# Performance work log

Hardware: AMD Instinct MI355X
Metric: run time of the kernel (lower is better)

## Reference

```python
import jax, jax.numpy as jnp
import numpy as np

E = 8          # num_experts
K = 2          # top_k
D = 1024       # hidden_size
I = 4096       # intermediate_size
AUX_COEF = 0.02


def setup_inputs() -> dict:
    key = jax.random.key(0)
    ks = jax.random.split(key, 5)
    x = jax.random.normal(ks[0], (4, 2048, D), dtype=jnp.float32)
    w_gate = jax.random.normal(ks[1], (E, D), dtype=jnp.float32) * 0.02   # router, nn.Linear weight [E, D]
    wg = jax.random.normal(ks[2], (E, D, I), dtype=jnp.float32) * 0.02    # gate_proj per expert
    wu = jax.random.normal(ks[3], (E, D, I), dtype=jnp.float32) * 0.02    # up_proj per expert
    wd = jax.random.normal(ks[4], (E, I, D), dtype=jnp.float32) * 0.02    # down_proj per expert
    return {"x": x, "w_gate": w_gate, "wg": wg, "wu": wu, "wd": wd}


def reference(x, w_gate, wg, wu, wd):
    B, T, Dm = x.shape
    xf = x.reshape(-1, Dm)                                   # [N, D]
    N = xf.shape[0]

    # 1) Router: softmax (in fp32) + top-k, renormalize top-k weights
    logits = xf @ w_gate.T                                   # [N, E]
    probs = jax.nn.softmax(logits.astype(jnp.float32), axis=-1)
    topk_w, topk_idx = jax.lax.top_k(probs, K)               # [N, K]
    topk_w = (topk_w / topk_w.sum(-1, keepdims=True)).astype(x.dtype)

    # Per-expert combine weight (zero when expert not selected) — math-equivalent
    # to the original gather/scatter-add loop but jit-friendly and vectorized.
    onehot = jax.nn.one_hot(topk_idx, E, dtype=x.dtype)      # [N, K, E]
    combine = jnp.einsum('nk,nke->ne', topk_w, onehot)       # [N, E]

    # 2) Experts: SwiGLU FFN, combined with routing weights
    out = jnp.zeros_like(xf)
    for e in range(E):  # fixed small loop over structurally distinct experts
        h = jax.nn.silu(xf @ wg[e]) * (xf @ wu[e])           # [N, I]
        out = out + combine[:, e:e + 1] * (h @ wd[e])        # [N, D]

    # 3) Load-balancing aux loss (Switch Transformer)
    f = onehot.sum((0, 1)).astype(jnp.float32) / (N * K)     # dispatch fraction per expert
    p = probs.mean(0)                                        # mean routing prob per expert
    aux_loss = AUX_COEF * E * jnp.sum(f * p)

    return out.reshape(B, T, Dm), aux_loss
```

## Files before the change

### kernel.cpp

```cpp
#include <hip/hip_runtime.h>
#include <hip/hip_bf16.h>
#include <cstdint>
#include <cstddef>

#define NE 8
#define TK 2
#define DM 1024
#define IM 4096
#define NT 8192
#define NS (NT*TK)
#define SCAP (NS+128)

typedef __bf16 bf16_t;
typedef __bf16 bf16x8 __attribute__((ext_vector_type(8)));
typedef __bf16 bf16x4 __attribute__((ext_vector_type(4)));
typedef float f32x4 __attribute__((ext_vector_type(4)));

__device__ __forceinline__ void async_cp16(const bf16_t* g, bf16_t* l) {
  __builtin_amdgcn_global_load_lds(
      (__attribute__((address_space(1))) void*)(const_cast<bf16_t*>(g)),
      (__attribute__((address_space(3))) void*)(l), 16, 0, 0);
}

__global__ void transpose_cvt(const float* __restrict__ src, bf16_t* __restrict__ dst,
                              int R, int C) {
  __shared__ float t[32][33];
  int bx = blockIdx.x * 32, by = blockIdx.y * 32;
  size_t zb = (size_t)blockIdx.z * R * C;
  int tx = threadIdx.x, ty = threadIdx.y;
#pragma unroll
  for (int i = 0; i < 4; ++i)
    t[ty + i*8][tx] = src[zb + (size_t)(by + ty + i*8) * C + bx + tx];
  __syncthreads();
#pragma unroll
  for (int i = 0; i < 4; ++i)
    dst[zb + (size_t)(bx + ty + i*8) * R + by + tx] = (bf16_t)t[tx][ty + i*8];
}

__global__ void router_kernel(const float* __restrict__ x, const float* __restrict__ wgate,
                              int* __restrict__ counts, float* __restrict__ prob_sum,
                              int* __restrict__ topk_idx, float* __restrict__ topk_w) {
  __shared__ float s_psum[NE];
  __shared__ int s_cnt[NE];
  int tid = threadIdx.x;
  if (tid < NE) { s_psum[tid] = 0.f; s_cnt[tid] = 0; }
  __syncthreads();
  int lane = tid & 63, wv = tid >> 6;
  for (int t = 0; t < 8; ++t) {
    int n = blockIdx.x * 32 + wv * 8 + t;
    float acc[NE];
#pragma unroll
    for (int e = 0; e < NE; ++e) acc[e] = 0.f;
#pragma unroll
    for (int j = 0; j < 16; ++j) {
      int d = j * 64 + lane;
      float xv = x[(size_t)n * DM + d];
#pragma unroll
      for (int e = 0; e < NE; ++e) acc[e] += xv * wgate[e * DM + d];
    }
#pragma unroll
    for (int e = 0; e < NE; ++e) {
#pragma unroll
      for (int off = 32; off > 0; off >>= 1) acc[e] += __shfl_xor(acc[e], off);
    }
    if (lane == 0) {
      float mx = acc[0];
#pragma unroll
      for (int e = 1; e < NE; ++e) mx = fmaxf(mx, acc[e]);
      float p[NE], s = 0.f;
#pragma unroll
      for (int e = 0; e < NE; ++e) { p[e] = __expf(acc[e] - mx); s += p[e]; }
      float inv = 1.f / s;
#pragma unroll
      for (int e = 0; e < NE; ++e) p[e] *= inv;
      int i0 = 0;
      for (int e = 1; e < NE; ++e) if (p[e] > p[i0]) i0 = e;
      int i1 = (i0 == 0) ? 1 : 0;
      for (int e = 0; e < NE; ++e) if (e != i0 && p[e] > p[i1]) i1 = e;
      float rs = 1.f / (p[i0] + p[i1]);
      topk_idx[n * 2 + 0] = i0; topk_idx[n * 2 + 1] = i1;
      topk_w[n * 2 + 0] = p[i0] * rs; topk_w[n * 2 + 1] = p[i1] * rs;
      atomicAdd(&s_cnt[i0], 1); atomicAdd(&s_cnt[i1], 1);
#pragma unroll
      for (int e = 0; e < NE; ++e) atomicAdd(&s_psum[e], p[e]);
    }
  }
  __syncthreads();
  if (tid < NE) { atomicAdd(&counts[tid], s_cnt[tid]); atomicAdd(&prob_sum[tid], s_psum[tid]); }
}

__global__ void scan_aux(const int* __restrict__ counts, const float* __restrict__ prob_sum,
                         int* __restrict__ offsets, int* __restrict__ cursors,
                         float* __restrict__ aux_out) {
  if (threadIdx.x == 0) {
    int off = 0;
    float aux = 0.f;
    for (int e = 0; e < NE; ++e) {
      offsets[e] = off; cursors[e] = off;
      float f = (float)counts[e] * (1.f / (float)NS);
      float p = prob_sum[e] * (1.f / (float)NT);
      aux += f * p;
      off += counts[e];
    }
    offsets[NE] = off;
    *aux_out = 0.02f * 8.f * aux;
  }
}

__global__ void gather_kernel(const float* __restrict__ x, const int* __restrict__ topk_idx,
                              const float* __restrict__ topk_w, int* __restrict__ cursors,
                              int* __restrict__ slot_token, float* __restrict__ slot_w,
                              int* __restrict__ pair_slot, bf16_t* __restrict__ Xg) {
  int lane = threadIdx.x & 63, wv = threadIdx.x >> 6;
  int pair = blockIdx.x * 4 + wv;
  int n = pair >> 1, k = pair & 1;
  int e = topk_idx[n * 2 + k];
  int slot = 0;
  if (lane == 0) slot = atomicAdd(&cursors[e], 1);
  slot = __shfl(slot, 0);
  if (lane == 0) {
    slot_token[slot] = n; slot_w[slot] = topk_w[n * 2 + k];
    pair_slot[pair] = slot;
  }
#pragma unroll
  for (int j = 0; j < 16; ++j) {
    int d = j * 64 + lane;
    Xg[(size_t)slot * DM + d] = (bf16_t)x[(size_t)n * DM + d];
  }
}

__global__ __launch_bounds__(256, 2) void gemm1_kernel(
    const bf16_t* __restrict__ Xg, const bf16_t* __restrict__ Wgt,
    const bf16_t* __restrict__ Wut, bf16_t* __restrict__ H,
    const int* __restrict__ offsets) {
  int e = blockIdx.z, mt = blockIdx.y, nt = blockIdx.x;
  int row0 = offsets[e], ne = offsets[e + 1] - row0;
  if (mt * 128 >= ne) return;
  int m0 = row0 + mt * 128;
  int n0 = nt * 128;

  __shared__ bf16_t sA[128 * 64];
  __shared__ bf16_t sG[128 * 64];
  __shared__ bf16_t sU[128 * 64];

  int tid = threadIdx.x, lane = tid & 63, wv = tid >> 6;
  int fm = lane & 15, fq = lane >> 4;
  int wm = (wv & 1) * 64, wn = (wv >> 1) * 64;

  f32x4 accg[4][4], accu[4][4];
#pragma unroll
  for (int i = 0; i < 4; ++i)
#pragma unroll
    for (int j = 0; j < 4; ++j) {
      accg[i][j] = (f32x4){0.f, 0.f, 0.f, 0.f};
      accu[i][j] = (f32x4){0.f, 0.f, 0.f, 0.f};
    }

  const bf16_t* Ab = Xg + (size_t)m0 * DM;
  const bf16_t* Gb = Wgt + ((size_t)e * IM + n0) * DM;
  const bf16_t* Ub = Wut + ((size_t)e * IM + n0) * DM;

  for (int k0 = 0; k0 < DM; k0 += 64) {
    __syncthreads();
#pragma unroll
    for (int it = 0; it < 4; ++it) {
      int c = it * 256 + tid;
      int r = c >> 3, c8 = c & 7;
      int gc8 = c8 ^ (r & 7);
      size_t go = (size_t)r * DM + k0 + gc8 * 8;
      async_cp16(Ab + go, sA + c * 8);
      async_cp16(Gb + go, sG + c * 8);
      async_cp16(Ub + go, sU + c * 8);
    }
    __syncthreads();
#pragma unroll
    for (int s = 0; s < 2; ++s) {
      bf16x8 af[4], gf[4], uf[4];
      int q = s * 4 + fq;
#pragma unroll
      for (int i = 0; i < 4; ++i) {
        int ra = wm + i * 16 + fm;
        int rb = wn + i * 16 + fm;
        af[i] = *(const bf16x8*)(sA + ra * 64 + (q ^ (ra & 7)) * 8);
        gf[i] = *(const bf16x8*)(sG + rb * 64 + (q ^ (rb & 7)) * 8);
        uf[i] = *(const bf16x8*)(sU + rb * 64 + (q ^ (rb & 7)) * 8);
      }
#pragma unroll
      for (int i = 0; i < 4; ++i)
#pragma unroll
        for (int j = 0; j < 4; ++j) {
          accg[i][j] = __builtin_amdgcn_mfma_f32_16x16x32_bf16(af[i], gf[j], accg[i][j], 0, 0, 0);
          accu[i][j] = __builtin_amdgcn_mfma_f32_16x16x32_bf16(af[i], uf[j], accu[i][j], 0, 0, 0);
        }
    }
  }
#pragma unroll
  for (int i = 0; i < 4; ++i) {
#pragma unroll
    for (int r = 0; r < 4; ++r) {
      int lm = wm + i * 16 + fq * 4 + r;
      if (mt * 128 + lm < ne) {
        bf16_t* hrow = H + (size_t)(m0 + lm) * IM + n0 + wn;
#pragma unroll
        for (int j = 0; j < 4; ++j) {
          float g = accg[i][j][r], u = accu[i][j][r];
          float h = g * __builtin_amdgcn_rcpf(1.f + __expf(-g)) * u;
          hrow[j * 16 + fm] = (bf16_t)h;
        }
      }
    }
  }
}

__global__ __launch_bounds__(256, 2) void gemm2_kernel(
    const bf16_t* __restrict__ H, const bf16_t* __restrict__ Wdt,
    const int* __restrict__ offsets, bf16_t* __restrict__ Y) {
  int e = blockIdx.z, mt = blockIdx.y, nt = blockIdx.x;
  int row0 = offsets[e], ne = offsets[e + 1] - row0;
  if (mt * 128 >= ne) return;
  int m0 = row0 + mt * 128;
  int n0 = nt * 128;

  __shared__ bf16_t sA[128 * 64];
  __shared__ bf16_t sB[128 * 64];

  int tid = threadIdx.x, lane = tid & 63, wv = tid >> 6;
  int fm = lane & 15, fq = lane >> 4;
  int wm = (wv & 1) * 64, wn = (wv >> 1) * 64;

  f32x4 acc[4][4];
#pragma unroll
  for (int i = 0; i < 4; ++i)
#pragma unroll
    for (int j = 0; j < 4; ++j) acc[i][j] = (f32x4){0.f, 0.f, 0.f, 0.f};

  const bf16_t* Ab = H + (size_t)m0 * IM;
  const bf16_t* Bb = Wdt + ((size_t)e * DM + n0) * IM;

  for (int k0 = 0; k0 < IM; k0 += 64) {
    __syncthreads();
#pragma unroll
    for (int it = 0; it < 4; ++it) {
      int c = it * 256 + tid;
      int r = c >> 3, c8 = c & 7;
      int gc8 = c8 ^ (r & 7);
      size_t go = (size_t)r * IM + k0 + gc8 * 8;
      async_cp16(Ab + go, sA + c * 8);
      async_cp16(Bb + go, sB + c * 8);
    }
    __syncthreads();
#pragma unroll
    for (int s = 0; s < 2; ++s) {
      bf16x8 af[4], bf[4];
      int q = s * 4 + fq;
#pragma unroll
      for (int i = 0; i < 4; ++i) {
        int ra = wm + i * 16 + fm;
        int rb = wn + i * 16 + fm;
        af[i] = *(const bf16x8*)(sA + ra * 64 + (q ^ (ra & 7)) * 8);
        bf[i] = *(const bf16x8*)(sB + rb * 64 + (q ^ (rb & 7)) * 8);
      }
#pragma unroll
      for (int i = 0; i < 4; ++i)
#pragma unroll
        for (int j = 0; j < 4; ++j)
          acc[i][j] = __builtin_amdgcn_mfma_f32_16x16x32_bf16(af[i], bf[j], acc[i][j], 0, 0, 0);
    }
  }
#pragma unroll
  for (int i = 0; i < 4; ++i) {
#pragma unroll
    for (int r = 0; r < 4; ++r) {
      int lm = wm + i * 16 + fq * 4 + r;
      if (mt * 128 + lm < ne) {
        bf16_t* yrow = Y + (size_t)(m0 + lm) * DM + n0 + wn;
#pragma unroll
        for (int j = 0; j < 4; ++j)
          yrow[j * 16 + fm] = (bf16_t)acc[i][j][r];
      }
    }
  }
}

__global__ void combine_kernel(const bf16_t* __restrict__ Y, const int* __restrict__ pair_slot,
                               const float* __restrict__ topk_w, float* __restrict__ out) {
  int n = blockIdx.x;
  int t = threadIdx.x;
  int s0 = pair_slot[n * 2 + 0], s1 = pair_slot[n * 2 + 1];
  float w0 = topk_w[n * 2 + 0], w1 = topk_w[n * 2 + 1];
  bf16x4 y0 = *(const bf16x4*)(Y + (size_t)s0 * DM + t * 4);
  bf16x4 y1 = *(const bf16x4*)(Y + (size_t)s1 * DM + t * 4);
  float4 o;
  o.x = w0 * (float)y0[0] + w1 * (float)y1[0];
  o.y = w0 * (float)y0[1] + w1 * (float)y1[1];
  o.z = w0 * (float)y0[2] + w1 * (float)y1[2];
  o.w = w0 * (float)y0[3] + w1 * (float)y1[3];
  *(float4*)(out + (size_t)n * DM + t * 4) = o;
}

static constexpr size_t OFF_TOPKI = 256;
static constexpr size_t OFF_TOPKW = OFF_TOPKI + (size_t)NT * 2 * 4;
static constexpr size_t OFF_STOK  = OFF_TOPKW + (size_t)NT * 2 * 4;
static constexpr size_t OFF_SW    = OFF_STOK + (size_t)NS * 4;
static constexpr size_t OFF_PSLOT = OFF_SW + (size_t)NS * 4;
static constexpr size_t OFF_XG    = OFF_PSLOT + (size_t)NS * 4;
static constexpr size_t OFF_H     = OFF_XG + (size_t)SCAP * DM * 2;
static constexpr size_t OFF_WGT   = OFF_H + (size_t)SCAP * IM * 2;
static constexpr size_t OFF_WUT   = OFF_WGT + (size_t)NE * IM * DM * 2;
static constexpr size_t OFF_WDT   = OFF_WUT + (size_t)NE * IM * DM * 2;

extern "C" void kernel_launch(void* const* d_in, const int* in_sizes, int n_in,
                              void* d_out, int out_size, void* d_ws, size_t ws_size,
                              hipStream_t stream) {
  const float* x      = (const float*)d_in[0];
  const float* w_gate = (const float*)d_in[1];
  const float* wg     = (const float*)d_in[2];
  const float* wu     = (const float*)d_in[3];
  const float* wd     = (const float*)d_in[4];
  float* out = (float*)d_out;

  char* ws = (char*)d_ws;
  int*   counts   = (int*)(ws + 0);
  int*   cursors  = (int*)(ws + 32);
  int*   offsets  = (int*)(ws + 64);
  float* prob_sum = (float*)(ws + 128);
  int*   topk_idx = (int*)(ws + OFF_TOPKI);
  float* topk_w   = (float*)(ws + OFF_TOPKW);
  int*   slot_tok = (int*)(ws + OFF_STOK);
  float* slot_w   = (float*)(ws + OFF_SW);
  int*   pair_slot= (int*)(ws + OFF_PSLOT);
  bf16_t* Xg  = (bf16_t*)(ws + OFF_XG);
  bf16_t* Yb  = Xg;
  bf16_t* Hb  = (bf16_t*)(ws + OFF_H);
  bf16_t* Wgt = (bf16_t*)(ws + OFF_WGT);
  bf16_t* Wut = (bf16_t*)(ws + OFF_WUT);
  bf16_t* Wdt = (bf16_t*)(ws + OFF_WDT);

  hipMemsetAsync(ws, 0, 256, stream);

  transpose_cvt<<<dim3(IM / 32, DM / 32, NE), dim3(32, 8), 0, stream>>>(wg, Wgt, DM, IM);
  transpose_cvt<<<dim3(IM / 32, DM / 32, NE), dim3(32, 8), 0, stream>>>(wu, Wut, DM, IM);
  transpose_cvt<<<dim3(DM / 32, IM / 32, NE), dim3(32, 8), 0, stream>>>(wd, Wdt, IM, DM);

  router_kernel<<<NT / 32, 256, 0, stream>>>(x, w_gate, counts, prob_sum, topk_idx, topk_w);
  scan_aux<<<1, 64, 0, stream>>>(counts, prob_sum, offsets, cursors, out + (out_size - 1));
  gather_kernel<<<NS / 4, 256, 0, stream>>>(x, topk_idx, topk_w, cursors, slot_tok, slot_w,
                                            pair_slot, Xg);

  gemm1_kernel<<<dim3(IM / 128, 64, NE), 256, 0, stream>>>(Xg, Wgt, Wut, Hb, offsets);
  gemm2_kernel<<<dim3(DM / 128, 64, NE), 256, 0, stream>>>(Hb, Wdt, offsets, Yb);
  combine_kernel<<<NT, 256, 0, stream>>>(Yb, pair_slot, topk_w, out);
}
```

Before: 1.241 ms.

## Rewrite gate/up GEMM as 256x256 double-buffered 8-wave kernel with packed weights

Gate and up weights are packed into one interleaved bf16 matrix, so each 256-column B tile holds 128 gate and 128 up columns. The gate/up GEMM now uses 512 threads, 256x256 tiles, double-buffered LDS, async global-to-LDS staging and explicit waitcnt, barrier and setprio scheduling to overlap loads with MFMA. The gather kernel also switches to float4 vectorized loads. Exchanges: a large LDS footprint (128 KB) that limits occupancy, more hand-tuned synchronization risk, and a 64-row grid dimension that still launches many empty blocks.

```diff
diff --git a/kernel.cpp b/kernel.cpp
--- a/kernel.cpp
+++ b/kernel.cpp
@@ -9,7 +9,7 @@
 #define IM 4096
 #define NT 8192
 #define NS (NT*TK)
-#define SCAP (NS+128)
+#define SCAP (NS+256)
 
 typedef __bf16 bf16_t;
 typedef __bf16 bf16x8 __attribute__((ext_vector_type(8)));
@@ -35,6 +35,26 @@
 #pragma unroll
   for (int i = 0; i < 4; ++i)
     dst[zb + (size_t)(bx + ty + i*8) * R + by + tx] = (bf16_t)t[tx][ty + i*8];
+}
+
+__global__ void pack_gu(const float* __restrict__ wg, const float* __restrict__ wu,
+                        bf16_t* __restrict__ Wgu) {
+  __shared__ float t[32][33];
+  int sel = blockIdx.z & 1, e = blockIdx.z >> 1;
+  const float* src = sel ? wu : wg;
+  size_t zb = (size_t)e * DM * IM;
+  int bx = blockIdx.x * 32, by = blockIdx.y * 32;
+  int tx = threadIdx.x, ty = threadIdx.y;
+#pragma unroll
+  for (int i = 0; i < 4; ++i)
+    t[ty + i*8][tx] = src[zb + (size_t)(by + ty + i*8) * IM + bx + tx];
+  __syncthreads();
+#pragma unroll
+  for (int i = 0; i < 4; ++i) {
+    int icol = bx + ty + i*8;
+    int p = ((icol >> 6) << 7) + (sel << 6) + (icol & 63);
+    Wgu[((size_t)e * (2*IM) + p) * DM + by + tx] = (bf16_t)t[tx][ty + i*8];
+  }
 }
 
 __global__ void router_kernel(const float* __restrict__ x, const float* __restrict__ wgate,
@@ -123,90 +143,174 @@
     pair_slot[pair] = slot;
   }
 #pragma unroll
-  for (int j = 0; j < 16; ++j) {
-    int d = j * 64 + lane;
-    Xg[(size_t)slot * DM + d] = (bf16_t)x[(size_t)n * DM + d];
-  }
-}
-
-__global__ __launch_bounds__(256, 2) void gemm1_kernel(
-    const bf16_t* __restrict__ Xg, const bf16_t* __restrict__ Wgt,
-    const bf16_t* __restrict__ Wut, bf16_t* __restrict__ H,
-    const int* __restrict__ offsets) {
+  for (int j = 0; j < 4; ++j) {
+    int d4 = j * 256 + lane * 4;
+    float4 v = *(const float4*)(x + (size_t)n * DM + d4);
+    bf16x4 o;
+    o[0] = (bf16_t)v.x; o[1] = (bf16_t)v.y; o[2] = (bf16_t)v.z; o[3] = (bf16_t)v.w;
+    *(bf16x4*)(Xg + (size_t)slot * DM + d4) = o;
+  }
+}
+
+#define MFMA16 __builtin_amdgcn_mfma_f32_16x16x32_bf16
+
+__global__ __launch_bounds__(512, 2) void gemm1_kernel(
+    const bf16_t* __restrict__ Xg, const bf16_t* __restrict__ Wgu,
+    bf16_t* __restrict__ H, const int* __restrict__ offsets) {
   int e = blockIdx.z, mt = blockIdx.y, nt = blockIdx.x;
   int row0 = offsets[e], ne = offsets[e + 1] - row0;
-  if (mt * 128 >= ne) return;
-  int m0 = row0 + mt * 128;
-  int n0 = nt * 128;
-
-  __shared__ bf16_t sA[128 * 64];
-  __shared__ bf16_t sG[128 * 64];
-  __shared__ bf16_t sU[128 * 64];
+  if (mt * 256 >= ne) return;
+  int m0 = row0 + mt * 256;
+
+  __shared__ bf16_t lds[2][4][128 * 64];
 
   int tid = threadIdx.x, lane = tid & 63, wv = tid >> 6;
   int fm = lane & 15, fq = lane >> 4;
-  int wm = (wv & 1) * 64, wn = (wv >> 1) * 64;
-
-  f32x4 accg[4][4], accu[4][4];
-#pragma unroll
-  for (int i = 0; i < 4; ++i)
-#pragma unroll
-    for (int j = 0; j < 4; ++j) {
-      accg[i][j] = (f32x4){0.f, 0.f, 0.f, 0.f};
-      accu[i][j] = (f32x4){0.f, 0.f, 0.f, 0.f};
-    }
+  int wm = wv >> 2, wn = wv & 3;
 
   const bf16_t* Ab = Xg + (size_t)m0 * DM;
-  const bf16_t* Gb = Wgt + ((size_t)e * IM + n0) * DM;
-  const bf16_t* Ub = Wut + ((size_t)e * IM + n0) * DM;
-
-  for (int k0 = 0; k0 < DM; k0 += 64) {
-    __syncthreads();
-#pragma unroll
-    for (int it = 0; it < 4; ++it) {
-      int c = it * 256 + tid;
-      int r = c >> 3, c8 = c & 7;
-      int gc8 = c8 ^ (r & 7);
-      size_t go = (size_t)r * DM + k0 + gc8 * 8;
-      async_cp16(Ab + go, sA + c * 8);
-      async_cp16(Gb + go, sG + c * 8);
-      async_cp16(Ub + go, sU + c * 8);
-    }
-    __syncthreads();
-#pragma unroll
-    for (int s = 0; s < 2; ++s) {
-      bf16x8 af[4], gf[4], uf[4];
-      int q = s * 4 + fq;
-#pragma unroll
-      for (int i = 0; i < 4; ++i) {
-        int ra = wm + i * 16 + fm;
-        int rb = wn + i * 16 + fm;
-        af[i] = *(const bf16x8*)(sA + ra * 64 + (q ^ (ra & 7)) * 8);
-        gf[i] = *(const bf16x8*)(sG + rb * 64 + (q ^ (rb & 7)) * 8);
-        uf[i] = *(const bf16x8*)(sU + rb * 64 + (q ^ (rb & 7)) * 8);
-      }
-#pragma unroll
-      for (int i = 0; i < 4; ++i)
-#pragma unroll
-        for (int j = 0; j < 4; ++j) {
-          accg[i][j] = __builtin_amdgcn_mfma_f32_16x16x32_bf16(af[i], gf[j], accg[i][j], 0, 0, 0);
-          accu[i][j] = __builtin_amdgcn_mfma_f32_16x16x32_bf16(af[i], uf[j], accu[i][j], 0, 0, 0);
-        }
-    }
-  }
-#pragma unroll
-  for (int i = 0; i < 4; ++i) {
-#pragma unroll
-    for (int r = 0; r < 4; ++r) {
-      int lm = wm + i * 16 + fq * 4 + r;
-      if (mt * 128 + lm < ne) {
-        bf16_t* hrow = H + (size_t)(m0 + lm) * IM + n0 + wn;
-#pragma unroll
-        for (int j = 0; j < 4; ++j) {
-          float g = accg[i][j][r], u = accu[i][j][r];
-          float h = g * __builtin_amdgcn_rcpf(1.f + __expf(-g)) * u;
-          hrow[j * 16 + fm] = (bf16_t)h;
-        }
+  const bf16_t* Bb = Wgu + ((size_t)e * (2 * IM) + nt * 256) * DM;
+
+  int sr = tid >> 3;
+  int sgc = ((tid & 7) ^ (sr & 7)) << 3;
+  int sldo = tid * 8;
+
+#define STAGE1(LDST, GBASE, COL) do {                                      \
+    const bf16_t* _g = (GBASE);                                            \
+    async_cp16(_g + (size_t)sr * DM + (COL) + sgc, (LDST) + sldo);         \
+    async_cp16(_g + (size_t)(sr + 64) * DM + (COL) + sgc, (LDST) + sldo + 4096); \
+  } while (0)
+
+  int offA[4][2], offB[2][2];
+#pragma unroll
+  for (int m = 0; m < 4; ++m) {
+    int r = m * 32 + wm * 16 + fm;
+#pragma unroll
+    for (int ks = 0; ks < 2; ++ks)
+      offA[m][ks] = r * 64 + (((ks * 4 + fq) ^ (r & 7)) << 3);
+  }
+#pragma unroll
+  for (int jh = 0; jh < 2; ++jh) {
+    int r = jh * 64 + wn * 16 + fm;
+#pragma unroll
+    for (int ks = 0; ks < 2; ++ks)
+      offB[jh][ks] = r * 64 + (((ks * 4 + fq) ^ (r & 7)) << 3);
+  }
+
+  f32x4 acc[8][4];
+#pragma unroll
+  for (int i = 0; i < 8; ++i)
+#pragma unroll
+    for (int j = 0; j < 4; ++j) acc[i][j] = (f32x4){0.f, 0.f, 0.f, 0.f};
+
+  STAGE1(lds[0][0], Ab, 0);
+  STAGE1(lds[0][2], Bb, 0);
+  STAGE1(lds[0][3], Bb + (size_t)128 * DM, 0);
+  STAGE1(lds[0][1], Ab + (size_t)128 * DM, 0);
+  STAGE1(lds[1][0], Ab, 64);
+  STAGE1(lds[1][2], Bb, 64);
+  STAGE1(lds[1][3], Bb + (size_t)128 * DM, 64);
+  asm volatile("s_waitcnt vmcnt(6)");
+  __builtin_amdgcn_s_barrier();
+
+  bf16x8 af[4][2], b0f[2][2], b1f[2][2];
+#pragma unroll 1
+  for (int t = 0; t < 16; ++t) {
+    const int buf = t & 1;
+    const bf16_t* LA0 = lds[buf][0];
+    const bf16_t* LA1 = lds[buf][1];
+    const bf16_t* LB0 = lds[buf][2];
+    const bf16_t* LB1 = lds[buf][3];
+#pragma unroll
+    for (int m = 0; m < 4; ++m) {
+      af[m][0] = *(const bf16x8*)(LA0 + offA[m][0]);
+      af[m][1] = *(const bf16x8*)(LA0 + offA[m][1]);
+    }
+#pragma unroll
+    for (int j = 0; j < 2; ++j) {
+      b0f[j][0] = *(const bf16x8*)(LB0 + offB[j][0]);
+      b0f[j][1] = *(const bf16x8*)(LB0 + offB[j][1]);
+    }
+    if (t + 1 < 16) STAGE1(lds[buf ^ 1][1], Ab + (size_t)128 * DM, (t + 1) * 64);
+    __builtin_amdgcn_s_barrier();
+    asm volatile("s_waitcnt lgkmcnt(0)");
+    __builtin_amdgcn_sched_barrier(0);
+    __builtin_amdgcn_s_setprio(1);
+#pragma unroll
+    for (int m = 0; m < 4; ++m)
+#pragma unroll
+      for (int j = 0; j < 2; ++j) {
+        acc[m][j] = MFMA16(af[m][0], b0f[j][0], acc[m][j], 0, 0, 0);
+        acc[m][j] = MFMA16(af[m][1], b0f[j][1], acc[m][j], 0, 0, 0);
+      }
+    __builtin_amdgcn_s_setprio(0);
+    __builtin_amdgcn_s_barrier();
+#pragma unroll
+    for (int j = 0; j < 2; ++j) {
+      b1f[j][0] = *(const bf16x8*)(LB1 + offB[j][0]);
+      b1f[j][1] = *(const bf16x8*)(LB1 + offB[j][1]);
+    }
+    if (t + 2 < 16) STAGE1(lds[buf][0], Ab, (t + 2) * 64);
+    __builtin_amdgcn_s_barrier();
+    asm volatile("s_waitcnt lgkmcnt(0)");
+    __builtin_amdgcn_sched_barrier(0);
+    __builtin_amdgcn_s_setprio(1);
+#pragma unroll
+    for (int m = 0; m < 4; ++m)
+#pragma unroll
+      for (int j = 0; j < 2; ++j) {
+        acc[m][2 + j] = MFMA16(af[m][0], b1f[j][0], acc[m][2 + j], 0, 0, 0);
+        acc[m][2 + j] = MFMA16(af[m][1], b1f[j][1], acc[m][2 + j], 0, 0, 0);
+      }
+    __builtin_amdgcn_s_setprio(0);
+    __builtin_amdgcn_s_barrier();
+#pragma unroll
+    for (int m = 0; m < 4; ++m) {
+      af[m][0] = *(const bf16x8*)(LA1 + offA[m][0]);
+      af[m][1] = *(const bf16x8*)(LA1 + offA[m][1]);
+    }
+    if (t + 2 < 16) STAGE1(lds[buf][2], Bb, (t + 2) * 64);
+    __builtin_amdgcn_s_barrier();
+    asm volatile("s_waitcnt lgkmcnt(0)");
+    __builtin_amdgcn_sched_barrier(0);
+    __builtin_amdgcn_s_setprio(1);
+#pragma unroll
+    for (int m = 0; m < 4; ++m)
+#pragma unroll
+      for (int j = 0; j < 2; ++j) {
+        acc[4 + m][j] = MFMA16(af[m][0], b0f[j][0], acc[4 + m][j], 0, 0, 0);
+        acc[4 + m][j] = MFMA16(af[m][1], b0f[j][1], acc[4 + m][j], 0, 0, 0);
+      }
+    __builtin_amdgcn_s_setprio(0);
+    __builtin_amdgcn_s_barrier();
+    if (t + 2 < 16) STAGE1(lds[buf][3], Bb + (size_t)128 * DM, (t + 2) * 64);
+    if (t < 14) { asm volatile("s_waitcnt vmcnt(6)"); }
+    else if (t == 14) { asm volatile("s_waitcnt vmcnt(0)"); }
+    __builtin_amdgcn_s_barrier();
+    __builtin_amdgcn_s_setprio(1);
+#pragma unroll
+    for (int m = 0; m < 4; ++m)
+#pragma unroll
+      for (int j = 0; j < 2; ++j) {
+        acc[4 + m][2 + j] = MFMA16(af[m][0], b1f[j][0], acc[4 + m][2 + j], 0, 0, 0);
+        acc[4 + m][2 + j] = MFMA16(af[m][1], b1f[j][1], acc[4 + m][2 + j], 0, 0, 0);
+      }
+    __builtin_amdgcn_s_setprio(0);
+    __builtin_amdgcn_s_barrier();
+  }
+#undef STAGE1
+
+#pragma unroll
+  for (int i = 0; i < 8; ++i) {
+    int lr = i * 32 + wm * 16 + fq * 4;
+#pragma unroll
+    for (int rr = 0; rr < 4; ++rr) {
+      if (mt * 256 + lr + rr < ne) {
+        bf16_t* hp = H + (size_t)(m0 + lr + rr) * IM + nt * 128 + wn * 16 + fm;
+        float g0 = acc[i][0][rr], u0 = acc[i][1][rr];
+        hp[0] = (bf16_t)(g0 * __builtin_amdgcn_rcpf(1.f + __expf(-g0)) * u0);
+        float g1 = acc[i][2][rr], u1 = acc[i][3][rr];
+        hp[64] = (bf16_t)(g1 * __builtin_amdgcn_rcpf(1.f + __expf(-g1)) * u1);
       }
     }
   }
@@ -305,9 +409,8 @@
 static constexpr size_t OFF_PSLOT = OFF_SW + (size_t)NS * 4;
 static constexpr size_t OFF_XG    = OFF_PSLOT + (size_t)NS * 4;
 static constexpr size_t OFF_H     = OFF_XG + (size_t)SCAP * DM * 2;
-static constexpr size_t OFF_WGT   = OFF_H + (size_t)SCAP * IM * 2;
-static constexpr size_t OFF_WUT   = OFF_WGT + (size_t)NE * IM * DM * 2;
-static constexpr size_t OFF_WDT   = OFF_WUT + (size_t)NE * IM * DM * 2;
+static constexpr size_t OFF_WGU   = OFF_H + (size_t)SCAP * IM * 2;
+static constexpr size_t OFF_WDT   = OFF_WGU + (size_t)NE * 2 * IM * DM * 2;
 
 extern "C" void kernel_launch(void* const* d_in, const int* in_sizes, int n_in,
                               void* d_out, int out_size, void* d_ws, size_t ws_size,
@@ -332,14 +435,12 @@
   bf16_t* Xg  = (bf16_t*)(ws + OFF_XG);
   bf16_t* Yb  = Xg;
   bf16_t* Hb  = (bf16_t*)(ws + OFF_H);
-  bf16_t* Wgt = (bf16_t*)(ws + OFF_WGT);
-  bf16_t* Wut = (bf16_t*)(ws + OFF_WUT);
+  bf16_t* Wgu = (bf16_t*)(ws + OFF_WGU);
   bf16_t* Wdt = (bf16_t*)(ws + OFF_WDT);
 
   hipMemsetAsync(ws, 0, 256, stream);
 
-  transpose_cvt<<<dim3(IM / 32, DM / 32, NE), dim3(32, 8), 0, stream>>>(wg, Wgt, DM, IM);
-  transpose_cvt<<<dim3(IM / 32, DM / 32, NE), dim3(32, 8), 0, stream>>>(wu, Wut, DM, IM);
+  pack_gu<<<dim3(IM / 32, DM / 32, NE * 2), dim3(32, 8), 0, stream>>>(wg, wu, Wgu);
   transpose_cvt<<<dim3(DM / 32, IM / 32, NE), dim3(32, 8), 0, stream>>>(wd, Wdt, IM, DM);
 
   router_kernel<<<NT / 32, 256, 0, stream>>>(x, w_gate, counts, prob_sum, topk_idx, topk_w);
@@ -347,7 +448,7 @@
   gather_kernel<<<NS / 4, 256, 0, stream>>>(x, topk_idx, topk_w, cursors, slot_tok, slot_w,
                                             pair_slot, Xg);
 
-  gemm1_kernel<<<dim3(IM / 128, 64, NE), 256, 0, stream>>>(Xg, Wgt, Wut, Hb, offsets);
+  gemm1_kernel<<<dim3(IM / 128, 64, NE), 512, 0, stream>>>(Xg, Wgu, Hb, offsets);
   gemm2_kernel<<<dim3(DM / 128, 64, NE), 256, 0, stream>>>(Hb, Wdt, offsets, Yb);
   combine_kernel<<<NT, 256, 0, stream>>>(Yb, pair_slot, topk_w, out);
 }
```

New measurement: 1.234 ms. Within noise of the previous version (-0.5%).
